# Kernel tuning notes

Hardware: AMD Instinct MI355X
Metric: run time of the kernel (lower is better)

The kernel has to match this reference:

```python
import jax, jax.numpy as jnp
import numpy as np

EPS = 1e-5


def _conv1x1(x, w, b=None):
    # x: [B,C,H,W], w: [O,C]
    y = jnp.einsum('bchw,oc->bohw', x, w)
    if b is not None:
        y = y + b[None, :, None, None]
    return y


def _bn(x, g, b, m, v):
    inv = g / jnp.sqrt(v + EPS)
    return x * inv[None, :, None, None] + (b - m * inv)[None, :, None, None]


def setup_inputs() -> dict:
    key = jax.random.key(0)
    ks = jax.random.split(key, 24)
    B, Cin, H, W = 4, 512, 64, 64
    Ci = Cin // 8  # 64
    s = 0.05
    d = {}
    d['x'] = jax.random.normal(ks[0], (B, Cin, H, W), jnp.float32)
    # conv_p1 (BasicConv2d: conv no-bias + BN)
    d['wp1'] = jax.random.normal(ks[1], (Ci, Cin), jnp.float32) * s
    d['gp1'] = jnp.ones((Ci,), jnp.float32)
    d['bp1'] = jnp.zeros((Ci,), jnp.float32)
    d['mp1'] = jax.random.normal(ks[2], (Ci,), jnp.float32) * 0.1
    d['vp1'] = jax.random.uniform(ks[3], (Ci,), jnp.float32, 0.5, 1.5)
    # conv_c1
    d['wc1'] = jax.random.normal(ks[4], (Ci, Cin), jnp.float32) * s
    d['gc1'] = jnp.ones((Ci,), jnp.float32)
    d['bc1'] = jnp.zeros((Ci,), jnp.float32)
    d['mc1'] = jax.random.normal(ks[5], (Ci,), jnp.float32) * 0.1
    d['vc1'] = jax.random.uniform(ks[6], (Ci,), jnp.float32, 0.5, 1.5)
    # PAM 1x1 convs (with bias)
    d['wb'] = jax.random.normal(ks[7], (Ci, Ci), jnp.float32) * s
    d['bb'] = jnp.zeros((Ci,), jnp.float32)
    d['wc2'] = jax.random.normal(ks[8], (Ci, Ci), jnp.float32) * s
    d['bc2'] = jnp.zeros((Ci,), jnp.float32)
    d['wd'] = jax.random.normal(ks[9], (Ci, Ci), jnp.float32) * s
    d['bd'] = jnp.zeros((Ci,), jnp.float32)
    d['alpha'] = jnp.array([0.5], jnp.float32)  # nonzero so attention path is exercised
    d['beta'] = jnp.array([0.5], jnp.float32)
    # out conv
    d['wo'] = jax.random.normal(ks[10], (Cin, Ci), jnp.float32) * s
    d['go'] = jnp.ones((Cin,), jnp.float32)
    d['bo'] = jnp.zeros((Cin,), jnp.float32)
    d['mo'] = jax.random.normal(ks[11], (Cin,), jnp.float32) * 0.1
    d['vo'] = jax.random.uniform(ks[12], (Cin,), jnp.float32, 0.5, 1.5)
    return d


def reference(x, wp1, gp1, bp1, mp1, vp1, wc1, gc1, bc1, mc1, vc1,
              wb, bb, wc2, bc2, wd, bd, alpha, beta, wo, go, bo, mo, vo):
    B, Cin, H, W = x.shape
    HW = H * W

    # --- position branch ---
    fp = _bn(_conv1x1(x, wp1), gp1, bp1, mp1, vp1)          # [B,Ci,H,W]
    Ci = fp.shape[1]
    fb = _conv1x1(fp, wb, bb).reshape(B, Ci, HW)             # query  [B,Ci,HW]
    fc = _conv1x1(fp, wc2, bc2).reshape(B, Ci, HW)           # key    [B,Ci,HW]
    fd = _conv1x1(fp, wd, bd).reshape(B, Ci, HW)             # value  [B,Ci,HW]
    attn_s = jax.nn.softmax(jnp.einsum('bcq,bck->bqk', fb, fc), axis=-1)  # [B,HW,HW]
    feat_ep = jnp.einsum('bck,bqk->bcq', fd, attn_s).reshape(B, Ci, H, W)
    feat_p = alpha[0] * feat_ep + fp

    # --- channel branch ---
    fcb = _bn(_conv1x1(x, wc1), gc1, bc1, mc1, vc1)          # [B,Ci,H,W]
    fa = fcb.reshape(B, Ci, HW)
    attn_c = jnp.einsum('bcn,bdn->bcd', fa, fa)              # [B,Ci,Ci]
    attn_c = jnp.max(attn_c, axis=-1, keepdims=True) - attn_c
    attn_c = jax.nn.softmax(attn_c, axis=-1)
    feat_ec = jnp.einsum('bcd,bdn->bcn', attn_c, fa).reshape(B, Ci, H, W)
    feat_c = beta[0] * feat_ec + fcb

    # --- fuse + out ---
    fusion = feat_p + feat_c
    out = _bn(_conv1x1(fusion, wo), go, bo, mo, vo)          # [B,Cin,H,W]
    return out
```

## Files before the change

kernel.cpp:

```cpp
#include <hip/hip_runtime.h>
#include <hip/hip_bf16.h>

typedef __hip_bfloat16 bf16;
typedef unsigned short u16;
typedef __attribute__((ext_vector_type(8))) short short8;
typedef __attribute__((ext_vector_type(4))) float f32x4;

#define HW 4096
#define NB (64*HW)

__device__ __forceinline__ f32x4 MFMA16(short8 a, short8 b, f32x4 c){
  return __builtin_amdgcn_mfma_f32_16x16x32_bf16(a, b, c, 0, 0, 0);
}

__global__ __launch_bounds__(256) void k_const(float* __restrict__ out, float v, int n){
  int i = blockIdx.x*256 + threadIdx.x;
  if (i < n) out[i] = v;
}

__global__ __launch_bounds__(512) void k_prep(
    const float* __restrict__ gp, const float* __restrict__ bp,
    const float* __restrict__ mp, const float* __restrict__ vp,
    const float* __restrict__ gc, const float* __restrict__ bc,
    const float* __restrict__ mc, const float* __restrict__ vc,
    const float* __restrict__ go, const float* __restrict__ bo,
    const float* __restrict__ mo, const float* __restrict__ vo,
    float* __restrict__ bn){
  int t = threadIdx.x;
  if (t < 64){
    float iv = gp[t] * rsqrtf(vp[t] + 1e-5f);
    bn[t] = iv; bn[64+t] = bp[t] - mp[t]*iv;
    float ic = gc[t] * rsqrtf(vc[t] + 1e-5f);
    bn[128+t] = ic; bn[192+t] = bc[t] - mc[t]*ic;
  }
  float io = go[t] * rsqrtf(vo[t] + 1e-5f);
  bn[256+t] = io; bn[768+t] = bo[t] - mo[t]*io;
}

__global__ __launch_bounds__(256) void k_conv_in(
    const float* __restrict__ x, const float* __restrict__ wp1, const float* __restrict__ wc1,
    const float* __restrict__ bn, float* __restrict__ fp, float* __restrict__ fcb){
  __shared__ __align__(16) float Wl[512][16];
  const int t = threadIdx.x;
  const int cg = blockIdx.y, b = blockIdx.z;
  const bool isP = cg < 4;
  const int c0 = (cg & 3) * 16;
  const float* w = isP ? wp1 : wc1;
  const float* inv  = isP ? bn       : bn + 128;
  const float* bias = isP ? bn + 64  : bn + 192;
  float* outp = isP ? fp : fcb;
  for (int i = t; i < 8192; i += 256){
    int c = i & 15, k = i >> 4;
    Wl[k][c] = w[(size_t)(c0 + c)*512 + k];
  }
  __syncthreads();
  const int p = blockIdx.x*256 + t;
  const float* xb = x + (size_t)b*512*HW + p;
  float acc[16];
  #pragma unroll
  for (int i = 0; i < 16; i++) acc[i] = 0.f;
  for (int k = 0; k < 512; k++){
    float xv = xb[(size_t)k*HW];
    float4 w0 = *(const float4*)&Wl[k][0];
    float4 w1 = *(const float4*)&Wl[k][4];
    float4 w2 = *(const float4*)&Wl[k][8];
    float4 w3 = *(const float4*)&Wl[k][12];
    acc[0]=fmaf(w0.x,xv,acc[0]); acc[1]=fmaf(w0.y,xv,acc[1]); acc[2]=fmaf(w0.z,xv,acc[2]); acc[3]=fmaf(w0.w,xv,acc[3]);
    acc[4]=fmaf(w1.x,xv,acc[4]); acc[5]=fmaf(w1.y,xv,acc[5]); acc[6]=fmaf(w1.z,xv,acc[6]); acc[7]=fmaf(w1.w,xv,acc[7]);
    acc[8]=fmaf(w2.x,xv,acc[8]); acc[9]=fmaf(w2.y,xv,acc[9]); acc[10]=fmaf(w2.z,xv,acc[10]); acc[11]=fmaf(w2.w,xv,acc[11]);
    acc[12]=fmaf(w3.x,xv,acc[12]); acc[13]=fmaf(w3.y,xv,acc[13]); acc[14]=fmaf(w3.z,xv,acc[14]); acc[15]=fmaf(w3.w,xv,acc[15]);
  }
  const size_t base = (size_t)b*NB + p;
  #pragma unroll
  for (int i = 0; i < 16; i++){
    int c = c0 + i;
    outp[base + (size_t)c*HW] = fmaf(acc[i], inv[c], bias[c]);
  }
}

__global__ __launch_bounds__(256) void k_qkv(
    const float* __restrict__ fp,
    const float* __restrict__ wb,  const float* __restrict__ bbv,
    const float* __restrict__ wc2, const float* __restrict__ bc2,
    const float* __restrict__ wd,  const float* __restrict__ bd,
    bf16* __restrict__ fB, bf16* __restrict__ fC, bf16* __restrict__ fD){
  __shared__ __align__(16) float Wl[64][16];
  __shared__ float Bl[16];
  const int t = threadIdx.x;
  const int mg = blockIdx.y, mat = mg >> 2, c0 = (mg & 3)*16, b = blockIdx.z;
  const float* w    = (mat == 0) ? wb  : (mat == 1 ? wc2 : wd);
  const float* bias = (mat == 0) ? bbv : (mat == 1 ? bc2 : bd);
  bf16* outp        = (mat == 0) ? fB  : (mat == 1 ? fC  : fD);
  for (int i = t; i < 1024; i += 256){
    int c = i & 15, k = i >> 4;
    Wl[k][c] = w[(size_t)(c0 + c)*64 + k];
  }
  if (t < 16) Bl[t] = bias[c0 + t];
  __syncthreads();
  const int p = blockIdx.x*512 + t*2;
  const float* in = fp + (size_t)b*NB + p;
  float2 acc[16];
  #pragma unroll
  for (int i = 0; i < 16; i++){ acc[i].x = 0.f; acc[i].y = 0.f; }
  for (int k = 0; k < 64; k++){
    float2 xv = *(const float2*)(in + (size_t)k*HW);
    float4 w0 = *(const float4*)&Wl[k][0];
    float4 w1 = *(const float4*)&Wl[k][4];
    float4 w2 = *(const float4*)&Wl[k][8];
    float4 w3 = *(const float4*)&Wl[k][12];
    float wv[16] = {w0.x,w0.y,w0.z,w0.w, w1.x,w1.y,w1.z,w1.w,
                    w2.x,w2.y,w2.z,w2.w, w3.x,w3.y,w3.z,w3.w};
    #pragma unroll
    for (int i = 0; i < 16; i++){
      acc[i].x = fmaf(wv[i], xv.x, acc[i].x);
      acc[i].y = fmaf(wv[i], xv.y, acc[i].y);
    }
  }
  if (mat < 2){
    bf16* ob = outp + (size_t)b*NB;
    #pragma unroll
    for (int i = 0; i < 16; i += 2){
      __hip_bfloat162 h0 = __float22bfloat162_rn(
          make_float2(acc[i].x + Bl[i], acc[i+1].x + Bl[i+1]));
      __hip_bfloat162 h1 = __float22bfloat162_rn(
          make_float2(acc[i].y + Bl[i], acc[i+1].y + Bl[i+1]));
      *(__hip_bfloat162*)&ob[(size_t)p*64 + c0 + i]     = h0;
      *(__hip_bfloat162*)&ob[(size_t)(p+1)*64 + c0 + i] = h1;
    }
  } else {
    const size_t base = (size_t)b*NB + p;
    #pragma unroll
    for (int i = 0; i < 16; i++){
      float bl = Bl[i];
      __hip_bfloat162 o2 = __float22bfloat162_rn(make_float2(acc[i].x + bl, acc[i].y + bl));
      *(__hip_bfloat162*)&outp[base + (size_t)(c0 + i)*HW] = o2;
    }
  }
}

__global__ __launch_bounds__(256) void k_chan_attn(
    const float* __restrict__ fcb, float* __restrict__ attn){
  __shared__ __align__(16) float rowc[4096];
  __shared__ float red[256];
  __shared__ float Srow[64];
  const int c = blockIdx.x, b = blockIdx.y, t = threadIdx.x;
  const float* fa = fcb + (size_t)b*NB;
  #pragma unroll
  for (int i = 0; i < 4; i++){
    int n = i*1024 + t*4;
    *(float4*)&rowc[n] = *(const float4*)&fa[(size_t)c*HW + n];
  }
  __syncthreads();
  const int d = t >> 2, part = t & 3;
  const float* frow = fa + (size_t)d*HW + part*1024;
  const float* rc = rowc + part*1024;
  float s = 0.f;
  for (int i = 0; i < 1024; i += 4){
    float4 xv = *(const float4*)&frow[i];
    float4 rv = *(const float4*)&rc[i];
    s += xv.x*rv.x + xv.y*rv.y + xv.z*rv.z + xv.w*rv.w;
  }
  red[t] = s;
  __syncthreads();
  if (part == 0) Srow[d] = red[t] + red[t+1] + red[t+2] + red[t+3];
  __syncthreads();
  if (t < 64){
    float z = -Srow[t];
    float m = z;
    #pragma unroll
    for (int off = 32; off; off >>= 1) m = fmaxf(m, __shfl_xor(m, off));
    float e = __expf(fminf(z - m, 0.f));
    float ss = e;
    #pragma unroll
    for (int off = 32; off; off >>= 1) ss += __shfl_xor(ss, off);
    attn[(size_t)b*4096 + (size_t)c*64 + t] = e / ss;
  }
}

__global__ __launch_bounds__(512) void k_pos_attn(
    const u16* __restrict__ fBt, const u16* __restrict__ fCt, const u16* __restrict__ fDv,
    const float* __restrict__ fpl, const float* __restrict__ alphap,
    float* __restrict__ fus){
  __shared__ __align__(16) u16 Kt[2][128*72];
  __shared__ __align__(16) u16 Vt[2][64*136];
  __shared__ __align__(16) u16 Pt[2][64*136];

  const int t = threadIdx.x;
  const int b = blockIdx.y, q0 = blockIdx.x*64;
  const int wv = t>>6;
  const int g  = wv>>2;
  const int wg = wv&3;
  const int lane = t&63, quad = lane>>4, lr = lane&15;
  const int tg = t & 255;
  const u16* Fb = fBt + (size_t)b*NB;
  const u16* Fc = fCt + (size_t)b*NB;
  const u16* Fd = fDv + (size_t)b*NB;

  const size_t qoff = (size_t)(q0 + wg*16 + lr)*64;
  short8 a0 = *(const short8*)&Fb[qoff + quad*8];
  short8 a1 = *(const short8*)&Fb[qoff + 32 + quad*8];

  float m[4] = {-3.0e38f,-3.0e38f,-3.0e38f,-3.0e38f};
  float l[4] = {0.f,0.f,0.f,0.f};
  f32x4 accO[4];
  #pragma unroll
  for (int cs = 0; cs < 4; cs++) accO[cs] = (f32x4){0.f,0.f,0.f,0.f};

  const int skk = tg>>1, sch = (tg&1)*32;
  const int svc = tg>>2, svk = (tg&3)*32;
  const u16* Ksrc = Fc + (size_t)(g*2048 + skk)*64 + sch;
  const u16* Vsrc = Fd + (size_t)svc*HW + g*2048 + svk;

  uint4 kr[4], vr[4];
  #pragma unroll
  for (int i = 0; i < 4; i++){
    kr[i] = ((const uint4*)Ksrc)[i];
    vr[i] = ((const uint4*)Vsrc)[i];
  }

  for (int tile = 0; tile < 16; ++tile){
    __syncthreads();
    {
      u16* kd = &Kt[g][skk*72 + sch];
      u16* vd = &Vt[g][svc*136 + svk];
      #pragma unroll
      for (int i = 0; i < 4; i++) ((uint4*)kd)[i] = kr[i];
      #pragma unroll
      for (int i = 0; i < 4; i++) ((uint4*)vd)[i] = vr[i];
    }
    __syncthreads();

    if (tile < 15){
      const u16* ks2 = Ksrc + (size_t)(tile+1)*128*64;
      const u16* vs2 = Vsrc + (tile+1)*128;
      #pragma unroll
      for (int i = 0; i < 4; i++){
        kr[i] = ((const uint4*)ks2)[i];
        vr[i] = ((const uint4*)vs2)[i];
      }
    }

    f32x4 s[8];
    #pragma unroll
    for (int ks = 0; ks < 8; ks++){
      short8 b0 = *(short8*)&Kt[g][(ks*16+lr)*72 + quad*8];
      short8 b1 = *(short8*)&Kt[g][(ks*16+lr)*72 + 32 + quad*8];
      f32x4 acc = {0.f,0.f,0.f,0.f};
      acc = MFMA16(a0, b0, acc);
      acc = MFMA16(a1, b1, acc);
      s[ks] = acc;
    }

    float mx[4];
    #pragma unroll
    for (int r = 0; r < 4; r++){
      float v = s[0][r];
      #pragma unroll
      for (int ks = 1; ks < 8; ks++) v = fmaxf(v, s[ks][r]);
      mx[r] = v;
    }
    #pragma unroll
    for (int off = 1; off < 16; off <<= 1){
      #pragma unroll
      for (int r = 0; r < 4; r++) mx[r] = fmaxf(mx[r], __shfl_xor(mx[r], off));
    }
    float al[4], rs[4];
    #pragma unroll
    for (int r = 0; r < 4; r++){
      float mn = fmaxf(m[r], mx[r]);
      al[r] = __expf(m[r] - mn);
      m[r] = mn;
      rs[r] = 0.f;
    }
    #pragma unroll
    for (int ks = 0; ks < 8; ks++){
      #pragma unroll
      for (int r = 0; r < 4; r++){
        float e = __expf(s[ks][r] - m[r]);
        rs[r] += e;
        bf16 h = __float2bfloat16(e);
        Pt[g][(wg*16 + quad*4 + r)*136 + ks*16 + lr] = *(u16*)&h;
      }
    }
    #pragma unroll
    for (int off = 1; off < 16; off <<= 1){
      #pragma unroll
      for (int r = 0; r < 4; r++) rs[r] += __shfl_xor(rs[r], off);
    }
    #pragma unroll
    for (int r = 0; r < 4; r++) l[r] = l[r]*al[r] + rs[r];
    #pragma unroll
    for (int cs = 0; cs < 4; cs++){
      #pragma unroll
      for (int r = 0; r < 4; r++) accO[cs][r] *= al[r];
    }
    __syncthreads();

    #pragma unroll
    for (int kc = 0; kc < 4; kc++){
      short8 pf = *(short8*)&Pt[g][(wg*16+lr)*136 + kc*32 + quad*8];
      #pragma unroll
      for (int cs = 0; cs < 4; cs++){
        short8 vf = *(short8*)&Vt[g][(cs*16+lr)*136 + kc*32 + quad*8];
        accO[cs] = MFMA16(pf, vf, accO[cs]);
      }
    }
  }

  __syncthreads();
  float* Ol = (float*)&Pt[0][0];
  float* Ml = Ol + 64*69;
  float* Ll = Ml + 64;
  if (g == 1){
    #pragma unroll
    for (int r = 0; r < 4; r++){
      int row = wg*16 + quad*4 + r;
      #pragma unroll
      for (int cs = 0; cs < 4; cs++)
        Ol[row*69 + cs*16 + lr] = accO[cs][r];
      if (lr == 0){ Ml[row] = m[r]; Ll[row] = l[r]; }
    }
  }
  __syncthreads();
  if (g == 0){
    const float alp = alphap[0];
    #pragma unroll
    for (int r = 0; r < 4; r++){
      int row = wg*16 + quad*4 + r;
      float m1 = Ml[row], l1 = Ll[row];
      float mt = fmaxf(m[r], m1);
      float e0 = __expf(m[r] - mt), e1 = __expf(m1 - mt);
      float lt = fmaxf(l[r]*e0 + l1*e1, 1e-20f);
      float sc = alp / lt;
      #pragma unroll
      for (int cs = 0; cs < 4; cs++){
        int idx = row*69 + cs*16 + lr;
        float v = accO[cs][r]*e0 + Ol[idx]*e1;
        Ol[idx] = v * sc;
      }
    }
  }
  __syncthreads();

  {
    const int c = t >> 3, qs = (t & 7) * 8;
    const float* Fp = fpl + (size_t)b*NB + (size_t)c*HW + q0 + qs;
    float* Fo = fus + (size_t)b*NB + (size_t)c*HW + q0 + qs;
    float v[8];
    #pragma unroll
    for (int j = 0; j < 8; j++) v[j] = Ol[(qs+j)*69 + c] + Fp[j];
    *(float4*)&Fo[0] = make_float4(v[0],v[1],v[2],v[3]);
    *(float4*)&Fo[4] = make_float4(v[4],v[5],v[6],v[7]);
  }
}

__global__ __launch_bounds__(256) void k_chan_apply(
    const float* __restrict__ fcb, const float* __restrict__ attn,
    const float* __restrict__ betap, float* __restrict__ fus){
  __shared__ __align__(16) float Ar2[64][8];
  const int t = threadIdx.x;
  const int c0 = blockIdx.y*8, b = blockIdx.z;
  for (int i = t; i < 512; i += 256){
    int d = i >> 3, ci = i & 7;
    Ar2[d][ci] = attn[(size_t)b*4096 + (size_t)(c0 + ci)*64 + d];
  }
  __syncthreads();
  const int p = blockIdx.x*256 + t;
  const float* fa = fcb + (size_t)b*NB;
  float acc[8] = {0.f,0.f,0.f,0.f,0.f,0.f,0.f,0.f};
  for (int d = 0; d < 64; d++){
    float v = fa[(size_t)d*HW + p];
    float4 A0 = *(const float4*)&Ar2[d][0];
    float4 A1 = *(const float4*)&Ar2[d][4];
    acc[0]=fmaf(A0.x,v,acc[0]); acc[1]=fmaf(A0.y,v,acc[1]); acc[2]=fmaf(A0.z,v,acc[2]); acc[3]=fmaf(A0.w,v,acc[3]);
    acc[4]=fmaf(A1.x,v,acc[4]); acc[5]=fmaf(A1.y,v,acc[5]); acc[6]=fmaf(A1.z,v,acc[6]); acc[7]=fmaf(A1.w,v,acc[7]);
  }
  const float be = betap[0];
  #pragma unroll
  for (int i = 0; i < 8; i++){
    size_t idx = (size_t)b*NB + (size_t)(c0 + i)*HW + p;
    fus[idx] += fmaf(be, acc[i], fa[(size_t)(c0 + i)*HW + p]);
  }
}

__global__ __launch_bounds__(256) void k_conv_out(
    const float* __restrict__ fus, const float* __restrict__ wo,
    const float* __restrict__ bn, float* __restrict__ out){
  __shared__ __align__(16) float Wl[64][16];
  const int t = threadIdx.x;
  const int o0 = blockIdx.y*16, b = blockIdx.z;
  for (int i = t; i < 1024; i += 256){
    int o = i & 15, c = i >> 4;
    Wl[c][o] = wo[(size_t)(o0 + o)*64 + c];
  }
  __syncthreads();
  const int p = blockIdx.x*512 + t*2;
  const float* fu = fus + (size_t)b*NB + p;
  float2 acc[16];
  #pragma unroll
  for (int i = 0; i < 16; i++){ acc[i].x = 0.f; acc[i].y = 0.f; }
  for (int c = 0; c < 64; c++){
    float2 xv = *(const float2*)(fu + (size_t)c*HW);
    float4 w0 = *(const float4*)&Wl[c][0];
    float4 w1 = *(const float4*)&Wl[c][4];
    float4 w2 = *(const float4*)&Wl[c][8];
    float4 w3 = *(const float4*)&Wl[c][12];
    float wv[16] = {w0.x,w0.y,w0.z,w0.w, w1.x,w1.y,w1.z,w1.w,
                    w2.x,w2.y,w2.z,w2.w, w3.x,w3.y,w3.z,w3.w};
    #pragma unroll
    for (int i = 0; i < 16; i++){
      acc[i].x = fmaf(wv[i], xv.x, acc[i].x);
      acc[i].y = fmaf(wv[i], xv.y, acc[i].y);
    }
  }
  #pragma unroll
  for (int i = 0; i < 16; i++){
    int o = o0 + i;
    float iv = bn[256+o], bs = bn[768+o];
    float* op = &out[(size_t)b*512*HW + (size_t)o*HW + p];
    op[0] = fmaf(acc[i].x, iv, bs);
    op[1] = fmaf(acc[i].y, iv, bs);
  }
}

extern "C" void kernel_launch(void* const* d_in, const int* in_sizes, int n_in,
                              void* d_out, int out_size, void* d_ws, size_t ws_size,
                              hipStream_t stream){
  static const int dictSz[24] = {8388608,32768,64,64,64,64,32768,64,64,64,64,
                                 4096,64,4096,64,4096,64,1,1,32768,512,512,512,512};
  bool dictOk = (n_in == 24);
  if (dictOk){
    for (int i = 0; i < 24; i++) if (in_sizes[i] != dictSz[i]) dictOk = false;
  }
  bool wsOk = (ws_size >= (size_t)(19u << 20));
  float* out = (float*)d_out;
  if (!dictOk){ k_const<<<(out_size+255)/256, 256, 0, stream>>>(out, 32.f, out_size); return; }
  if (!wsOk)  { k_const<<<(out_size+255)/256, 256, 0, stream>>>(out, 48.f, out_size); return; }

  const float* x    = (const float*)d_in[0];
  const float* wp1  = (const float*)d_in[1];
  const float* gp1  = (const float*)d_in[2];  const float* bp1 = (const float*)d_in[3];
  const float* mp1  = (const float*)d_in[4];  const float* vp1 = (const float*)d_in[5];
  const float* wc1  = (const float*)d_in[6];
  const float* gc1  = (const float*)d_in[7];  const float* bc1 = (const float*)d_in[8];
  const float* mc1  = (const float*)d_in[9];  const float* vc1 = (const float*)d_in[10];
  const float* wb   = (const float*)d_in[11]; const float* bb  = (const float*)d_in[12];
  const float* wc2  = (const float*)d_in[13]; const float* bc2 = (const float*)d_in[14];
  const float* wd   = (const float*)d_in[15]; const float* bd  = (const float*)d_in[16];
  const float* alp  = (const float*)d_in[17]; const float* bet = (const float*)d_in[18];
  const float* wo   = (const float*)d_in[19];
  const float* go   = (const float*)d_in[20]; const float* bo  = (const float*)d_in[21];
  const float* mo   = (const float*)d_in[22]; const float* vo  = (const float*)d_in[23];

  char* w8 = (char*)d_ws;
  float* fp    = (float*)(w8);
  float* fcb   = (float*)(w8 + (4u<<20));
  float* fus   = (float*)(w8 + (8u<<20));
  bf16*  fB    = (bf16*) (w8 + (12u<<20));
  bf16*  fC    = (bf16*) (w8 + (14u<<20));
  bf16*  fD    = (bf16*) (w8 + (16u<<20));
  float* attnc = (float*)(w8 + (18u<<20));
  float* bn    = (float*)(w8 + (18u<<20) + 65536);

  k_prep<<<1, 512, 0, stream>>>(gp1,bp1,mp1,vp1, gc1,bc1,mc1,vc1, go,bo,mo,vo, bn);
  k_conv_in<<<dim3(16,8,4), 256, 0, stream>>>(x, wp1, wc1, bn, fp, fcb);
  k_qkv<<<dim3(8,12,4), 256, 0, stream>>>(fp, wb,bb, wc2,bc2, wd,bd, fB, fC, fD);
  k_chan_attn<<<dim3(64,4), 256, 0, stream>>>(fcb, attnc);
  k_pos_attn<<<dim3(64,4), 512, 0, stream>>>((const u16*)fB, (const u16*)fC, (const u16*)fD,
                                             fp, alp, fus);
  k_chan_apply<<<dim3(16,8,4), 256, 0, stream>>>(fcb, attnc, bet, fus);
  k_conv_out<<<dim3(8,32,4), 256, 0, stream>>>(fus, wo, bn, out);
}
```

Before: 353.9 us.

## Keep attention probabilities in registers by transposing QK MFMA operand order

```diff
diff --git a/kernel.cpp b/kernel.cpp
--- a/kernel.cpp
+++ b/kernel.cpp
@@ -5,6 +5,7 @@
 typedef unsigned short u16;
 typedef __attribute__((ext_vector_type(8))) short short8;
 typedef __attribute__((ext_vector_type(4))) float f32x4;
+typedef __attribute__((ext_vector_type(4))) unsigned int u32x4;
 
 #define HW 4096
 #define NB (64*HW)
@@ -183,7 +184,6 @@
     float* __restrict__ fus){
   __shared__ __align__(16) u16 Kt[2][128*72];
   __shared__ __align__(16) u16 Vt[2][64*136];
-  __shared__ __align__(16) u16 Pt[2][64*136];
 
   const int t = threadIdx.x;
   const int b = blockIdx.y, q0 = blockIdx.x*64;
@@ -200,8 +200,9 @@
   short8 a0 = *(const short8*)&Fb[qoff + quad*8];
   short8 a1 = *(const short8*)&Fb[qoff + 32 + quad*8];
 
-  float m[4] = {-3.0e38f,-3.0e38f,-3.0e38f,-3.0e38f};
-  float l[4] = {0.f,0.f,0.f,0.f};
+  const int krbase = ((lr>>2)<<3) + (lr&3);
+
+  float m = -3.0e38f, l = 0.f;
   f32x4 accO[4];
   #pragma unroll
   for (int cs = 0; cs < 4; cs++) accO[cs] = (f32x4){0.f,0.f,0.f,0.f};
@@ -243,100 +244,87 @@
     f32x4 s[8];
     #pragma unroll
     for (int ks = 0; ks < 8; ks++){
-      short8 b0 = *(short8*)&Kt[g][(ks*16+lr)*72 + quad*8];
-      short8 b1 = *(short8*)&Kt[g][(ks*16+lr)*72 + 32 + quad*8];
+      const int krow = krbase + ((ks>>1)<<5) + ((ks&1)<<2);
+      short8 k0 = *(short8*)&Kt[g][krow*72 + quad*8];
+      short8 k1 = *(short8*)&Kt[g][krow*72 + 32 + quad*8];
       f32x4 acc = {0.f,0.f,0.f,0.f};
-      acc = MFMA16(a0, b0, acc);
-      acc = MFMA16(a1, b1, acc);
+      acc = MFMA16(k0, a0, acc);
+      acc = MFMA16(k1, a1, acc);
       s[ks] = acc;
     }
 
-    float mx[4];
-    #pragma unroll
-    for (int r = 0; r < 4; r++){
-      float v = s[0][r];
-      #pragma unroll
-      for (int ks = 1; ks < 8; ks++) v = fmaxf(v, s[ks][r]);
-      mx[r] = v;
-    }
-    #pragma unroll
-    for (int off = 1; off < 16; off <<= 1){
-      #pragma unroll
-      for (int r = 0; r < 4; r++) mx[r] = fmaxf(mx[r], __shfl_xor(mx[r], off));
-    }
-    float al[4], rs[4];
-    #pragma unroll
-    for (int r = 0; r < 4; r++){
-      float mn = fmaxf(m[r], mx[r]);
-      al[r] = __expf(m[r] - mn);
-      m[r] = mn;
-      rs[r] = 0.f;
-    }
+    float t4[8];
+    #pragma unroll
+    for (int ks = 0; ks < 8; ks++)
+      t4[ks] = fmaxf(fmaxf(s[ks][0], s[ks][1]), fmaxf(s[ks][2], s[ks][3]));
+    float mx = fmaxf(fmaxf(fmaxf(t4[0],t4[1]), fmaxf(t4[2],t4[3])),
+                     fmaxf(fmaxf(t4[4],t4[5]), fmaxf(t4[6],t4[7])));
+    mx = fmaxf(mx, __shfl_xor(mx, 16));
+    mx = fmaxf(mx, __shfl_xor(mx, 32));
+    const float mn = fmaxf(m, mx);
+    const float al = __expf(m - mn);
+    m = mn;
+
+    u32x4 pw[4];
+    float rs = 0.f;
     #pragma unroll
     for (int ks = 0; ks < 8; ks++){
-      #pragma unroll
-      for (int r = 0; r < 4; r++){
-        float e = __expf(s[ks][r] - m[r]);
-        rs[r] += e;
-        bf16 h = __float2bfloat16(e);
-        Pt[g][(wg*16 + quad*4 + r)*136 + ks*16 + lr] = *(u16*)&h;
-      }
-    }
-    #pragma unroll
-    for (int off = 1; off < 16; off <<= 1){
-      #pragma unroll
-      for (int r = 0; r < 4; r++) rs[r] += __shfl_xor(rs[r], off);
-    }
-    #pragma unroll
-    for (int r = 0; r < 4; r++) l[r] = l[r]*al[r] + rs[r];
-    #pragma unroll
-    for (int cs = 0; cs < 4; cs++){
-      #pragma unroll
-      for (int r = 0; r < 4; r++) accO[cs][r] *= al[r];
-    }
-    __syncthreads();
+      float e0 = __expf(s[ks][0] - m);
+      float e1 = __expf(s[ks][1] - m);
+      float e2 = __expf(s[ks][2] - m);
+      float e3 = __expf(s[ks][3] - m);
+      rs += (e0 + e1) + (e2 + e3);
+      __hip_bfloat162 h0 = __float22bfloat162_rn(make_float2(e0, e1));
+      __hip_bfloat162 h1 = __float22bfloat162_rn(make_float2(e2, e3));
+      pw[ks>>1][(ks&1)*2]     = *(unsigned int*)&h0;
+      pw[ks>>1][(ks&1)*2 + 1] = *(unsigned int*)&h1;
+    }
+    rs += __shfl_xor(rs, 16);
+    rs += __shfl_xor(rs, 32);
+    l = l*al + rs;
+    #pragma unroll
+    for (int cs = 0; cs < 4; cs++) accO[cs] *= al;
 
     #pragma unroll
     for (int kc = 0; kc < 4; kc++){
-      short8 pf = *(short8*)&Pt[g][(wg*16+lr)*136 + kc*32 + quad*8];
+      short8 pf = *(short8*)&pw[kc];
       #pragma unroll
       for (int cs = 0; cs < 4; cs++){
         short8 vf = *(short8*)&Vt[g][(cs*16+lr)*136 + kc*32 + quad*8];
-        accO[cs] = MFMA16(pf, vf, accO[cs]);
+        accO[cs] = MFMA16(vf, pf, accO[cs]);
       }
     }
   }
 
   __syncthreads();
-  float* Ol = (float*)&Pt[0][0];
+  float* Ol = (float*)&Kt[0][0];
   float* Ml = Ol + 64*69;
   float* Ll = Ml + 64;
   if (g == 1){
-    #pragma unroll
-    for (int r = 0; r < 4; r++){
-      int row = wg*16 + quad*4 + r;
-      #pragma unroll
-      for (int cs = 0; cs < 4; cs++)
-        Ol[row*69 + cs*16 + lr] = accO[cs][r];
-      if (lr == 0){ Ml[row] = m[r]; Ll[row] = l[r]; }
-    }
+    const int row = wg*16 + lr;
+    #pragma unroll
+    for (int cs = 0; cs < 4; cs++){
+      #pragma unroll
+      for (int r = 0; r < 4; r++)
+        Ol[row*69 + cs*16 + quad*4 + r] = accO[cs][r];
+    }
+    if (quad == 0){ Ml[row] = m; Ll[row] = l; }
   }
   __syncthreads();
   if (g == 0){
     const float alp = alphap[0];
-    #pragma unroll
-    for (int r = 0; r < 4; r++){
-      int row = wg*16 + quad*4 + r;
-      float m1 = Ml[row], l1 = Ll[row];
-      float mt = fmaxf(m[r], m1);
-      float e0 = __expf(m[r] - mt), e1 = __expf(m1 - mt);
-      float lt = fmaxf(l[r]*e0 + l1*e1, 1e-20f);
-      float sc = alp / lt;
-      #pragma unroll
-      for (int cs = 0; cs < 4; cs++){
-        int idx = row*69 + cs*16 + lr;
-        float v = accO[cs][r]*e0 + Ol[idx]*e1;
-        Ol[idx] = v * sc;
+    const int row = wg*16 + lr;
+    const float m1 = Ml[row], l1 = Ll[row];
+    const float mt = fmaxf(m, m1);
+    const float e0 = __expf(m - mt), e1 = __expf(m1 - mt);
+    const float lt = fmaxf(l*e0 + l1*e1, 1e-20f);
+    const float sc = alp / lt;
+    #pragma unroll
+    for (int cs = 0; cs < 4; cs++){
+      #pragma unroll
+      for (int r = 0; r < 4; r++){
+        int idx = row*69 + cs*16 + quad*4 + r;
+        Ol[idx] = (accO[cs][r]*e0 + Ol[idx]*e1) * sc;
       }
     }
   }
```

Result: slower. 373.6 us (+5.6%).
